# Kernel optimization log

Hardware: AMD Instinct MI355X
Metric: run time of the kernel (lower is better)

Reference implementation:

```python
import jax, jax.numpy as jnp
import numpy as np

N = 100000   # nodes
E = 640000   # edges
D = 128      # feature dim
G = 512      # graphs in the batch


def setup_inputs() -> dict:
    key = jax.random.key(0)
    ks = jax.random.split(key, 6)
    x = jax.random.normal(ks[0], (N, D), dtype=jnp.float32)
    edge_index = jax.random.randint(ks[1], (2, E), 0, N, dtype=jnp.int32)
    batch = jnp.sort(jax.random.randint(ks[2], (N,), 0, G, dtype=jnp.int32))
    scale = 1.0 / np.sqrt(D)
    W0 = jax.random.normal(ks[3], (D, D), dtype=jnp.float32) * scale
    W1 = jax.random.normal(ks[4], (D, D), dtype=jnp.float32) * scale
    W2 = jax.random.normal(ks[5], (D, D), dtype=jnp.float32) * scale
    return {"x": x, "edge_index": edge_index, "batch": batch,
            "W0": W0, "W1": W1, "W2": W2}


def gcn_conv(x, W, row, col, n):
    """GCNConv (bias=False): x' = D^-1/2 (A + I) D^-1/2 (x @ W).
    row/col already include self-loops."""
    xw = x @ W                                              # [N, D]
    deg = jax.ops.segment_sum(jnp.ones_like(col, dtype=x.dtype), col,
                              num_segments=n)               # [N]
    dinv = jnp.where(deg > 0, jax.lax.rsqrt(deg), 0.0)
    norm = dinv[row] * dinv[col]                            # [E+N]
    msgs = norm[:, None] * xw[row]                          # gather + scale
    return jax.ops.segment_sum(msgs, col, num_segments=n)   # scatter-add


def reference(x, edge_index, batch, W0, W1, W2):
    n = x.shape[0]
    loops = jnp.arange(n, dtype=edge_index.dtype)
    row = jnp.concatenate([edge_index[0], loops])
    col = jnp.concatenate([edge_index[1], loops])
    # conv_layers[:-1] (no activation between them in forward)
    x = gcn_conv(x, W0, row, col, n)
    x = gcn_conv(x, W1, row, col, n)
    x = jax.nn.leaky_relu(x, negative_slope=0.01)
    x = gcn_conv(x, W2, row, col, n)
    # global_add_pool over graph ids
    return jax.ops.segment_sum(x, batch, num_segments=G)    # [G, D]
```

## Files before the change

kernel.cpp:

```cpp
#include <hip/hip_runtime.h>
#include <hip/hip_bf16.h>

#define FEAT 128

typedef unsigned int uint32;
typedef unsigned short ushort16;
typedef __attribute__((ext_vector_type(8))) short short8;
typedef __attribute__((ext_vector_type(4))) float v4f;
typedef __attribute__((ext_vector_type(2))) float f32x2;

__device__ __forceinline__ ushort16 f2bf(float f) {
    uint32 u = __float_as_uint(f);
    u += 0x7fffu + ((u >> 16) & 1u);
    return (ushort16)(u >> 16);
}
__device__ __forceinline__ float bflo(uint32 u) { return __uint_as_float(u << 16); }
__device__ __forceinline__ float bfhi(uint32 u) { return __uint_as_float(u & 0xffff0000u); }
__device__ __forceinline__ f32x2 up2(uint32 u) { return (f32x2){bflo(u), bfhi(u)}; }

__device__ __forceinline__ void gemm_body(const float* __restrict__ A,
                                          const ushort16* __restrict__ Wt,
                                          ushort16* __restrict__ Ch, int n,
                                          int pairId, int pairStride,
                                          int tile0, int tile1, int t) {
    const int w = t >> 6;
    const int lane = t & 63;
    const int quad = lane >> 4;
    const int l16 = lane & 15;
    const int colBase = (w & 1) * 64;

    short8 wf[4][4];
#pragma unroll
    for (int ct = 0; ct < 4; ct++) {
        const ushort16* wp = Wt + (size_t)(colBase + ct * 16 + l16) * FEAT + quad * 8;
#pragma unroll
        for (int ks = 0; ks < 4; ks++) wf[ct][ks] = *(const short8*)(wp + ks * 32);
    }

    int tile = tile0 + pairId;
    if (tile >= tile1) return;

    auto loadA = [&](int tl, short8 (&a)[4]) {
        const int rowi = tl * 16 + l16;
        if (rowi < n) {
#pragma unroll
            for (int ks = 0; ks < 4; ks++) {
                const float* ap = A + (size_t)rowi * FEAT + quad * 8 + ks * 32;
                float4 f0 = *(const float4*)ap;
                float4 f1 = *(const float4*)(ap + 4);
                short8 v;
                v[0] = f2bf(f0.x); v[1] = f2bf(f0.y); v[2] = f2bf(f0.z); v[3] = f2bf(f0.w);
                v[4] = f2bf(f1.x); v[5] = f2bf(f1.y); v[6] = f2bf(f1.z); v[7] = f2bf(f1.w);
                a[ks] = v;
            }
        } else {
#pragma unroll
            for (int ks = 0; ks < 4; ks++) a[ks] = (short8)0;
        }
    };

    short8 aCur[4];
    loadA(tile, aCur);

    while (tile < tile1) {
        const int nextTile = tile + pairStride;
        short8 aNxt[4];
        if (nextTile < tile1) loadA(nextTile, aNxt);

        v4f acc[4];
#pragma unroll
        for (int ct = 0; ct < 4; ct++) acc[ct] = (v4f)0.f;
#pragma unroll
        for (int ct = 0; ct < 4; ct++)
#pragma unroll
            for (int ks = 0; ks < 4; ks++)
                acc[ct] = __builtin_amdgcn_mfma_f32_16x16x32_bf16(wf[ct][ks], aCur[ks], acc[ct], 0, 0, 0);

        const int rowi = tile * 16 + l16;
        if (rowi < n) {
#pragma unroll
            for (int ct = 0; ct < 4; ct++) {
                uint2 o;
                o.x = (uint32)f2bf(acc[ct][0]) | ((uint32)f2bf(acc[ct][1]) << 16);
                o.y = (uint32)f2bf(acc[ct][2]) | ((uint32)f2bf(acc[ct][3]) << 16);
                *(uint2*)(Ch + (size_t)rowi * FEAT + colBase + ct * 16 + quad * 4) = o;
            }
        }

        tile = nextTile;
#pragma unroll
        for (int ks = 0; ks < 4; ks++) aCur[ks] = aNxt[ks];
    }
}

__global__ __launch_bounds__(256) void pre_kernel(int* __restrict__ counts, int n,
                                                  const float* __restrict__ W0,
                                                  const float* __restrict__ W1,
                                                  ushort16* __restrict__ W01t,
                                                  float* __restrict__ Pbuf) {
    int b = blockIdx.x;
    int t = threadIdx.x;
    if (b < 100) {
        int idx = (b * 256 + t) * 4;
        if (idx + 3 < n) {
            *(int4*)(counts + idx) = make_int4(0, 0, 0, 0);
        } else {
            for (int i = idx; i < n; i++) counts[i] = 0;
        }
    } else if (b < 164) {
        __shared__ float sW0[2][FEAT];
        int wb = b - 100;
        int lk = t >> 7;
        int ncol = t & 127;
        int k = wb * 2 + lk;
        sW0[lk][ncol] = W0[(size_t)k * FEAT + ncol];
        __syncthreads();
        float acc = 0.f;
#pragma unroll 4
        for (int j = 0; j < FEAT; j++)
            acc += sW0[lk][j] * W1[(size_t)j * FEAT + ncol];
        W01t[(size_t)ncol * FEAT + k] = f2bf(acc);
    } else {
        int zb = b - 164;
        float4 z = make_float4(0.f, 0.f, 0.f, 0.f);
        float* p = Pbuf + (size_t)zb * 2048 + t * 8;
        *(float4*)p = z;
        *(float4*)(p + 4) = z;
    }
}

__global__ __launch_bounds__(256) void histgemmA_kernel(const int* __restrict__ col,
                                                        int* __restrict__ counts, int E,
                                                        const float* __restrict__ A,
                                                        const ushort16* __restrict__ Wt,
                                                        ushort16* __restrict__ Ch, int n) {
    const int b = blockIdx.x;
    const int r9 = b % 9;
    const int g9 = b / 9;
    const int t = threadIdx.x;
    if (r9 >= 4) {
        int hb = g9 * 5 + (r9 - 4);
        int id = hb * 256 + t;
        if (id * 4 + 3 < E) {
            int4 c4 = *(const int4*)(col + id * 4);
            atomicAdd(&counts[c4.x], 1);
            atomicAdd(&counts[c4.y], 1);
            atomicAdd(&counts[c4.z], 1);
            atomicAdd(&counts[c4.w], 1);
        } else {
            for (int e = id * 4; e < E; e++) atomicAdd(&counts[col[e]], 1);
        }
        return;
    }
    int gb = g9 * 4 + r9;
    gemm_body(A, Wt, Ch, n, gb * 2 + ((t >> 6) >> 1), 1024, 0, 3125, t);
}

__global__ __launch_bounds__(256) void scan_part(const int* __restrict__ counts,
                                                 int* __restrict__ bsum, int n) {
    __shared__ int s[256];
    int base = blockIdx.x * 1024;
    int t = threadIdx.x;
    int v = 0;
#pragma unroll
    for (int i = 0; i < 4; i++) {
        int idx = base + t * 4 + i;
        if (idx < n) v += counts[idx];
    }
    s[t] = v;
    __syncthreads();
    for (int o = 128; o > 0; o >>= 1) {
        if (t < o) s[t] += s[t + o];
        __syncthreads();
    }
    if (t == 0) bsum[blockIdx.x] = s[0];
}

__global__ __launch_bounds__(256) void scan_final(const int* __restrict__ counts,
                                                  const int* __restrict__ bsum,
                                                  int* __restrict__ off, int* __restrict__ nxt,
                                                  float* __restrict__ dinv, int n, int nb) {
    __shared__ int s[256];
    __shared__ int sb[128];
    int base = blockIdx.x * 1024;
    int t = threadIdx.x;
    if (t < nb) sb[t] = bsum[t];
    int c[4];
    int sum = 0;
#pragma unroll
    for (int i = 0; i < 4; i++) {
        int idx = base + t * 4 + i;
        c[i] = (idx < n) ? counts[idx] : 0;
        sum += c[i];
    }
    int v0 = sum;
    s[t] = sum;
    __syncthreads();
    for (int o = 1; o < 256; o <<= 1) {
        int v = (t >= o) ? s[t - o] : 0;
        __syncthreads();
        s[t] += v;
        __syncthreads();
    }
    int blockBase = 0;
    for (int j = 0; j < blockIdx.x; j++) blockBase += sb[j];
    int excl = s[t] - v0 + blockBase;
#pragma unroll
    for (int i = 0; i < 4; i++) {
        int idx = base + t * 4 + i;
        if (idx < n) {
            off[idx] = excl;
            nxt[idx] = excl;
            dinv[idx] = rsqrtf((float)(c[i] + 1));
        }
        excl += c[i];
    }
    if (blockIdx.x == gridDim.x - 1 && t == 255) off[n] = excl;
}

__global__ __launch_bounds__(256) void fillgemmB_kernel(const float* __restrict__ A,
                                                        const ushort16* __restrict__ Wt,
                                                        ushort16* __restrict__ Ch, int n,
                                                        const int* __restrict__ row,
                                                        const int* __restrict__ col,
                                                        int* __restrict__ nxt,
                                                        int* __restrict__ srcArr, int E) {
    const int b = blockIdx.x;
    const int r7 = b % 7;
    const int g7 = b / 7;
    const int t = threadIdx.x;
    if (r7 >= 2) {
        int fb = g7 * 5 + (r7 - 2);
        int e = fb * 256 + t;
        if (e < E) {
            int c = col[e], r = row[e];
            int p = atomicAdd(&nxt[c], 1);
            __builtin_nontemporal_store(r, &srcArr[p]);
        }
        return;
    }
    int gb = g7 * 2 + r7;
    gemm_body(A, Wt, Ch, n, gb * 2 + ((t >> 6) >> 1), 2048, 3125, 6250, t);
}

template <int MODE>
__global__ __launch_bounds__(256) void gather_kernel(const int* __restrict__ off,
                                                     const int* __restrict__ srcArr,
                                                     const float* __restrict__ dinv,
                                                     const uint4* __restrict__ table,
                                                     ushort16* __restrict__ Hh, int n) {
    const int t = threadIdx.x;
    const int node = blockIdx.x * 4 + (t >> 6);
    if (node >= n) return;
    const int lane = t & 63;
    const int grp = lane >> 4;
    const int l16 = lane & 15;
    float dc = dinv[node];

    f32x2 acc[4];
    if (grp == 0) {
        uint4 v = table[(size_t)node * 16 + l16];
        if (MODE == 0) {
            f32x2 w0 = (f32x2){dc, dc};
            acc[0] = w0 * up2(v.x);
            acc[1] = w0 * up2(v.y);
            acc[2] = w0 * up2(v.z);
            acc[3] = w0 * up2(v.w);
        } else {
            acc[0] = up2(v.x);
            acc[1] = up2(v.y);
            acc[2] = up2(v.z);
            acc[3] = up2(v.w);
        }
    } else {
#pragma unroll
        for (int j = 0; j < 4; j++) acc[j] = (f32x2){0.f, 0.f};
    }

    int s = off[node], e = off[node + 1];
    int i = s + grp;
    if (MODE == 0) {
        for (; i + 4 < e; i += 8) {
            int r0 = srcArr[i];
            int r1 = srcArr[i + 4];
            uint4 u0 = table[(size_t)r0 * 16 + l16];
            uint4 u1 = table[(size_t)r1 * 16 + l16];
            float f0 = dinv[r0];
            float f1 = dinv[r1];
            f32x2 n0 = (f32x2){f0, f0};
            f32x2 n1 = (f32x2){f1, f1};
            acc[0] += n0 * up2(u0.x);
            acc[1] += n0 * up2(u0.y);
            acc[2] += n0 * up2(u0.z);
            acc[3] += n0 * up2(u0.w);
            acc[0] += n1 * up2(u1.x);
            acc[1] += n1 * up2(u1.y);
            acc[2] += n1 * up2(u1.z);
            acc[3] += n1 * up2(u1.w);
        }
        if (i < e) {
            int r0 = srcArr[i];
            uint4 u0 = table[(size_t)r0 * 16 + l16];
            float f0 = dinv[r0];
            f32x2 n0 = (f32x2){f0, f0};
            acc[0] += n0 * up2(u0.x);
            acc[1] += n0 * up2(u0.y);
            acc[2] += n0 * up2(u0.z);
            acc[3] += n0 * up2(u0.w);
        }
    } else {
        for (; i + 4 < e; i += 8) {
            int r0 = srcArr[i];
            int r1 = srcArr[i + 4];
            uint4 u0 = table[(size_t)r0 * 16 + l16];
            uint4 u1 = table[(size_t)r1 * 16 + l16];
            acc[0] += up2(u0.x) + up2(u1.x);
            acc[1] += up2(u0.y) + up2(u1.y);
            acc[2] += up2(u0.z) + up2(u1.z);
            acc[3] += up2(u0.w) + up2(u1.w);
        }
        if (i < e) {
            int r0 = srcArr[i];
            uint4 u0 = table[(size_t)r0 * 16 + l16];
            acc[0] += up2(u0.x);
            acc[1] += up2(u0.y);
            acc[2] += up2(u0.z);
            acc[3] += up2(u0.w);
        }
    }

    float b[8] = {acc[0].x, acc[0].y, acc[1].x, acc[1].y,
                  acc[2].x, acc[2].y, acc[3].x, acc[3].y};
#pragma unroll
    for (int j = 0; j < 8; j++) {
        b[j] += __shfl_xor(b[j], 16);
        b[j] += __shfl_xor(b[j], 32);
    }

    if (grp == 0) {
        float sc = dc * dc;
        if (MODE == 1) {
#pragma unroll
            for (int j = 0; j < 8; j++) {
                float h = b[j];
                h = (h >= 0.f) ? h : 0.01f * h;
                b[j] = sc * h;
            }
        } else {
#pragma unroll
            for (int j = 0; j < 8; j++) b[j] *= sc;
        }
        uint4 o;
        o.x = (uint32)f2bf(b[0]) | ((uint32)f2bf(b[1]) << 16);
        o.y = (uint32)f2bf(b[2]) | ((uint32)f2bf(b[3]) << 16);
        o.z = (uint32)f2bf(b[4]) | ((uint32)f2bf(b[5]) << 16);
        o.w = (uint32)f2bf(b[6]) | ((uint32)f2bf(b[7]) << 16);
        *(uint4*)(Hh + (size_t)node * FEAT + l16 * 8) = o;
    }
}

__global__ __launch_bounds__(256) void gatherpool_kernel(const int* __restrict__ off,
                                                         const int* __restrict__ srcArr,
                                                         const float* __restrict__ dinv,
                                                         const uint4* __restrict__ table,
                                                         const int* __restrict__ batch,
                                                         float* __restrict__ P, int n) {
    const int t = threadIdx.x;
    const int wave = blockIdx.x * 4 + (t >> 6);
    const int lane = t & 63;
    const int grp = lane >> 4;
    const int l16 = lane & 15;

    const int node0 = wave * 16;
    if (node0 >= n) return;
    const int node1 = min(node0 + 16, n);

    float pacc[8];
#pragma unroll
    for (int j = 0; j < 8; j++) pacc[j] = 0.f;
    int cur = batch[node0];

    for (int node = node0; node < node1; node++) {
        float dc = dinv[node];
        f32x2 acc[4];
        if (grp == 0) {
            uint4 v = table[(size_t)node * 16 + l16];
            acc[0] = up2(v.x);
            acc[1] = up2(v.y);
            acc[2] = up2(v.z);
            acc[3] = up2(v.w);
        } else {
#pragma unroll
            for (int j = 0; j < 4; j++) acc[j] = (f32x2){0.f, 0.f};
        }

        int s = off[node], e = off[node + 1];
        int i = s + grp;
        for (; i + 4 < e; i += 8) {
            int r0 = srcArr[i];
            int r1 = srcArr[i + 4];
            uint4 u0 = table[(size_t)r0 * 16 + l16];
            uint4 u1 = table[(size_t)r1 * 16 + l16];
            acc[0] += up2(u0.x) + up2(u1.x);
            acc[1] += up2(u0.y) + up2(u1.y);
            acc[2] += up2(u0.z) + up2(u1.z);
            acc[3] += up2(u0.w) + up2(u1.w);
        }
        if (i < e) {
            int r0 = srcArr[i];
            uint4 u0 = table[(size_t)r0 * 16 + l16];
            acc[0] += up2(u0.x);
            acc[1] += up2(u0.y);
            acc[2] += up2(u0.z);
            acc[3] += up2(u0.w);
        }

        float b[8] = {acc[0].x, acc[0].y, acc[1].x, acc[1].y,
                      acc[2].x, acc[2].y, acc[3].x, acc[3].y};
#pragma unroll
        for (int j = 0; j < 8; j++) {
            b[j] += __shfl_xor(b[j], 16);
            b[j] += __shfl_xor(b[j], 32);
        }

        int g = batch[node];
        if (g != cur) {
            atomicAdd(&P[(size_t)cur * FEAT + l16 * 8 + 2 * grp], pacc[2 * grp]);
            atomicAdd(&P[(size_t)cur * FEAT + l16 * 8 + 2 * grp + 1], pacc[2 * grp + 1]);
#pragma unroll
            for (int j = 0; j < 8; j++) pacc[j] = 0.f;
            cur = g;
        }
#pragma unroll
        for (int j = 0; j < 8; j++) pacc[j] += dc * b[j];
    }
    atomicAdd(&P[(size_t)cur * FEAT + l16 * 8 + 2 * grp], pacc[2 * grp]);
    atomicAdd(&P[(size_t)cur * FEAT + l16 * 8 + 2 * grp + 1], pacc[2 * grp + 1]);
}

__global__ __launch_bounds__(128) void pgemm_kernel(const float* __restrict__ P,
                                                    const float* __restrict__ W2,
                                                    float* __restrict__ out) {
    __shared__ float sP[FEAT];
    const int g = blockIdx.x;
    const int t = threadIdx.x;
    sP[t] = P[(size_t)g * FEAT + t];
    __syncthreads();
    float o = 0.f;
#pragma unroll 4
    for (int k = 0; k < FEAT; k++) o += sP[k] * W2[(size_t)k * FEAT + t];
    out[(size_t)g * FEAT + t] = o;
}

extern "C" void kernel_launch(void* const* d_in, const int* in_sizes, int n_in,
                              void* d_out, int out_size, void* d_ws, size_t ws_size,
                              hipStream_t stream) {
    const float* x = (const float*)d_in[0];
    const int* ei = (const int*)d_in[1];
    const int* batch = (const int*)d_in[2];
    const float* W0 = (const float*)d_in[3];
    const float* W1 = (const float*)d_in[4];
    const float* W2 = (const float*)d_in[5];
    float* out = (float*)d_out;

    const int N = in_sizes[0] / FEAT;
    const int E = in_sizes[1] / 2;
    const int G = out_size / FEAT;

    const int* rowI = ei;
    const int* colI = ei + E;

    char* ws = (char*)d_ws;
    auto take = [&](size_t bytes) {
        char* p = ws;
        ws += (bytes + 15) & ~(size_t)15;
        return p;
    };
    int* counts    = (int*)take((size_t)N * 4);
    int* off       = (int*)take((size_t)(N + 1) * 4);
    int* nxt       = (int*)take((size_t)N * 4);
    float* dinv    = (float*)take((size_t)N * 4);
    int* bsum      = (int*)take(128 * 4);
    int* srcArr    = (int*)take((size_t)E * 4);
    ushort16* W01t = (ushort16*)take((size_t)16384 * 2);
    float* Pbuf    = (float*)take((size_t)G * FEAT * 4);
    ushort16* bufA = (ushort16*)take((size_t)N * FEAT * 2);
    ushort16* bufB = (ushort16*)take((size_t)N * FEAT * 2);

    const int nb = (N + 1023) / 1024;

    pre_kernel<<<196, 256, 0, stream>>>(counts, N, W0, W1, W01t, Pbuf);

    histgemmA_kernel<<<128 * 9, 256, 0, stream>>>(colI, counts, E, x, W01t, bufA, N);

    scan_part<<<nb, 256, 0, stream>>>(counts, bsum, N);
    scan_final<<<nb, 256, 0, stream>>>(counts, bsum, off, nxt, dinv, N, nb);

    fillgemmB_kernel<<<512 * 7, 256, 0, stream>>>(x, W01t, bufA, N,
                                                  rowI, colI, nxt, srcArr, E);

    const int gatBlocks = (N + 3) / 4;
    gather_kernel<0><<<gatBlocks, 256, 0, stream>>>(off, srcArr, dinv,
                                                    (const uint4*)bufA, bufB, N);
    gather_kernel<1><<<gatBlocks, 256, 0, stream>>>(off, srcArr, dinv,
                                                    (const uint4*)bufB, bufA, N);
    const int nWaves = (N + 15) / 16;
    const int poolBlocks = (nWaves + 3) / 4;
    gatherpool_kernel<<<poolBlocks, 256, 0, stream>>>(off, srcArr, dinv,
                                                      (const uint4*)bufA, batch,
                                                      Pbuf, N);
    pgemm_kernel<<<G, 128, 0, stream>>>(Pbuf, W2, out);
}
```

Measured before the change: 327.1 us.

## Fuse tail gathers into cooperative persistent kernel and chain-scan offsets

Replaces the two-kernel scan with a single decoupled chained scan: each block publishes its total through a flag array and the earlier blocks' totals are summed by spinning. The two gather passes, the pooled gather and the final small GEMM are merged into one cooperative persistent kernel of 2048 blocks, with grid-wide syncs in place of separate launches. The aim is to remove launch gaps and tail idle time between the small dependent stages. In exchange it adds grid-sync costs and a grid-stride loop. The chained scan relies on earlier blocks being scheduled first, and the fused path depends on the cooperative launch succeeding, with the old kernels kept as a fallback.

Result: slower. 1.075 ms (+228.5%).

```diff
diff --git a/kernel.cpp b/kernel.cpp
--- a/kernel.cpp
+++ b/kernel.cpp
@@ -1,5 +1,8 @@
 #include <hip/hip_runtime.h>
 #include <hip/hip_bf16.h>
+#include <hip/hip_cooperative_groups.h>
+
+namespace cg = cooperative_groups;
 
 #define FEAT 128
 
@@ -97,7 +100,8 @@
                                                   const float* __restrict__ W0,
                                                   const float* __restrict__ W1,
                                                   ushort16* __restrict__ W01t,
-                                                  float* __restrict__ Pbuf) {
+                                                  float* __restrict__ Pbuf,
+                                                  int* __restrict__ flagval) {
     int b = blockIdx.x;
     int t = threadIdx.x;
     if (b < 100) {
@@ -120,12 +124,14 @@
         for (int j = 0; j < FEAT; j++)
             acc += sW0[lk][j] * W1[(size_t)j * FEAT + ncol];
         W01t[(size_t)ncol * FEAT + k] = f2bf(acc);
-    } else {
+    } else if (b < 196) {
         int zb = b - 164;
         float4 z = make_float4(0.f, 0.f, 0.f, 0.f);
         float* p = Pbuf + (size_t)zb * 2048 + t * 8;
         *(float4*)p = z;
         *(float4*)(p + 4) = z;
+    } else {
+        if (t < 128) flagval[t] = 0;
     }
 }
 
@@ -156,35 +162,15 @@
     gemm_body(A, Wt, Ch, n, gb * 2 + ((t >> 6) >> 1), 1024, 0, 3125, t);
 }
 
-__global__ __launch_bounds__(256) void scan_part(const int* __restrict__ counts,
-                                                 int* __restrict__ bsum, int n) {
+__global__ __launch_bounds__(256) void scan_chain(const int* __restrict__ counts,
+                                                  int* __restrict__ flagval,
+                                                  int* __restrict__ off, int* __restrict__ nxt,
+                                                  float* __restrict__ dinv, int n) {
     __shared__ int s[256];
-    int base = blockIdx.x * 1024;
-    int t = threadIdx.x;
-    int v = 0;
-#pragma unroll
-    for (int i = 0; i < 4; i++) {
-        int idx = base + t * 4 + i;
-        if (idx < n) v += counts[idx];
-    }
-    s[t] = v;
-    __syncthreads();
-    for (int o = 128; o > 0; o >>= 1) {
-        if (t < o) s[t] += s[t + o];
-        __syncthreads();
-    }
-    if (t == 0) bsum[blockIdx.x] = s[0];
-}
-
-__global__ __launch_bounds__(256) void scan_final(const int* __restrict__ counts,
-                                                  const int* __restrict__ bsum,
-                                                  int* __restrict__ off, int* __restrict__ nxt,
-                                                  float* __restrict__ dinv, int n, int nb) {
-    __shared__ int s[256];
-    __shared__ int sb[128];
-    int base = blockIdx.x * 1024;
-    int t = threadIdx.x;
-    if (t < nb) sb[t] = bsum[t];
+    __shared__ int sBase;
+    const int b = blockIdx.x;
+    const int base = b * 1024;
+    const int t = threadIdx.x;
     int c[4];
     int sum = 0;
 #pragma unroll
@@ -202,9 +188,18 @@
         s[t] += v;
         __syncthreads();
     }
-    int blockBase = 0;
-    for (int j = 0; j < blockIdx.x; j++) blockBase += sb[j];
-    int excl = s[t] - v0 + blockBase;
+    if (t == 255) atomicExch(&flagval[b], s[255] + 1);
+    if (t == 0) {
+        int acc = 0;
+        for (int j = 0; j < b; j++) {
+            int v;
+            do { v = atomicAdd(&flagval[j], 0); } while (v == 0);
+            acc += v - 1;
+        }
+        sBase = acc;
+    }
+    __syncthreads();
+    int excl = s[t] - v0 + sBase;
 #pragma unroll
     for (int i = 0; i < 4; i++) {
         int idx = base + t * 4 + i;
@@ -215,7 +210,7 @@
         }
         excl += c[i];
     }
-    if (blockIdx.x == gridDim.x - 1 && t == 255) off[n] = excl;
+    if (b == gridDim.x - 1 && t == 255) off[n] = excl;
 }
 
 __global__ __launch_bounds__(256) void fillgemmB_kernel(const float* __restrict__ A,
@@ -244,19 +239,13 @@
 }
 
 template <int MODE>
-__global__ __launch_bounds__(256) void gather_kernel(const int* __restrict__ off,
-                                                     const int* __restrict__ srcArr,
-                                                     const float* __restrict__ dinv,
-                                                     const uint4* __restrict__ table,
-                                                     ushort16* __restrict__ Hh, int n) {
-    const int t = threadIdx.x;
-    const int node = blockIdx.x * 4 + (t >> 6);
-    if (node >= n) return;
-    const int lane = t & 63;
-    const int grp = lane >> 4;
-    const int l16 = lane & 15;
+__device__ __forceinline__ void gather_node_body(int node, int grp, int l16,
+                                                 const int* __restrict__ off,
+                                                 const int* __restrict__ srcArr,
+                                                 const float* __restrict__ dinv,
+                                                 const uint4* __restrict__ table,
+                                                 ushort16* __restrict__ Hh) {
     float dc = dinv[node];
-
     f32x2 acc[4];
     if (grp == 0) {
         uint4 v = table[(size_t)node * 16 + l16];
@@ -359,20 +348,14 @@
     }
 }
 
-__global__ __launch_bounds__(256) void gatherpool_kernel(const int* __restrict__ off,
-                                                         const int* __restrict__ srcArr,
-                                                         const float* __restrict__ dinv,
-                                                         const uint4* __restrict__ table,
-                                                         const int* __restrict__ batch,
-                                                         float* __restrict__ P, int n) {
-    const int t = threadIdx.x;
-    const int wave = blockIdx.x * 4 + (t >> 6);
-    const int lane = t & 63;
-    const int grp = lane >> 4;
-    const int l16 = lane & 15;
-
+__device__ __forceinline__ void gatherpool_wave(int wave, int grp, int l16,
+                                                const int* __restrict__ off,
+                                                const int* __restrict__ srcArr,
+                                                const float* __restrict__ dinv,
+                                                const uint4* __restrict__ table,
+                                                const int* __restrict__ batch,
+                                                float* __restrict__ P, int n) {
     const int node0 = wave * 16;
-    if (node0 >= n) return;
     const int node1 = min(node0 + 16, n);
 
     float pacc[8];
@@ -438,18 +421,87 @@
     atomicAdd(&P[(size_t)cur * FEAT + l16 * 8 + 2 * grp + 1], pacc[2 * grp + 1]);
 }
 
+__device__ __forceinline__ void pgemm_graph(int g, int t,
+                                            const float* __restrict__ P,
+                                            const float* __restrict__ W2,
+                                            float* __restrict__ out) {
+    __shared__ float sP[FEAT];
+    if (t < FEAT) sP[t] = P[(size_t)g * FEAT + t];
+    __syncthreads();
+    if (t < FEAT) {
+        float o = 0.f;
+#pragma unroll 4
+        for (int k = 0; k < FEAT; k++) o += sP[k] * W2[(size_t)k * FEAT + t];
+        out[(size_t)g * FEAT + t] = o;
+    }
+    __syncthreads();
+}
+
+template <int MODE>
+__global__ __launch_bounds__(256) void gather_kernel(const int* __restrict__ off,
+                                                     const int* __restrict__ srcArr,
+                                                     const float* __restrict__ dinv,
+                                                     const uint4* __restrict__ table,
+                                                     ushort16* __restrict__ Hh, int n) {
+    const int t = threadIdx.x;
+    const int node = blockIdx.x * 4 + (t >> 6);
+    if (node >= n) return;
+    gather_node_body<MODE>(node, (t & 63) >> 4, t & 15, off, srcArr, dinv, table, Hh);
+}
+
+__global__ __launch_bounds__(256) void gatherpool_kernel(const int* __restrict__ off,
+                                                         const int* __restrict__ srcArr,
+                                                         const float* __restrict__ dinv,
+                                                         const uint4* __restrict__ table,
+                                                         const int* __restrict__ batch,
+                                                         float* __restrict__ P, int n) {
+    const int t = threadIdx.x;
+    const int wave = blockIdx.x * 4 + (t >> 6);
+    if (wave * 16 >= n) return;
+    gatherpool_wave(wave, (t & 63) >> 4, t & 15, off, srcArr, dinv, table, batch, P, n);
+}
+
 __global__ __launch_bounds__(128) void pgemm_kernel(const float* __restrict__ P,
                                                     const float* __restrict__ W2,
                                                     float* __restrict__ out) {
-    __shared__ float sP[FEAT];
-    const int g = blockIdx.x;
+    pgemm_graph(blockIdx.x, threadIdx.x, P, W2, out);
+}
+
+__global__ __launch_bounds__(256, 8) void tail_kernel(const int* __restrict__ off,
+                                                      const int* __restrict__ srcArr,
+                                                      const float* __restrict__ dinv,
+                                                      ushort16* __restrict__ bufA,
+                                                      ushort16* __restrict__ bufB,
+                                                      const int* __restrict__ batch,
+                                                      float* __restrict__ P,
+                                                      const float* __restrict__ W2,
+                                                      float* __restrict__ out,
+                                                      int n, int G) {
+    cg::grid_group grid = cg::this_grid();
     const int t = threadIdx.x;
-    sP[t] = P[(size_t)g * FEAT + t];
-    __syncthreads();
-    float o = 0.f;
-#pragma unroll 4
-    for (int k = 0; k < FEAT; k++) o += sP[k] * W2[(size_t)k * FEAT + t];
-    out[(size_t)g * FEAT + t] = o;
+    const int grp = (t & 63) >> 4;
+    const int l16 = t & 15;
+
+    for (int q = blockIdx.x; q * 4 < n; q += gridDim.x) {
+        int node = q * 4 + (t >> 6);
+        if (node < n)
+            gather_node_body<0>(node, grp, l16, off, srcArr, dinv,
+                                (const uint4*)bufA, bufB);
+    }
+    grid.sync();
+    for (int q = blockIdx.x; q * 4 < n; q += gridDim.x) {
+        int node = q * 4 + (t >> 6);
+        if (node < n)
+            gather_node_body<1>(node, grp, l16, off, srcArr, dinv,
+                                (const uint4*)bufB, bufA);
+    }
+    grid.sync();
+    for (int wave = blockIdx.x * 4 + (t >> 6); wave * 16 < n; wave += gridDim.x * 4)
+        gatherpool_wave(wave, grp, l16, off, srcArr, dinv,
+                        (const uint4*)bufA, batch, P, n);
+    grid.sync();
+    for (int g = blockIdx.x; g < G; g += gridDim.x)
+        pgemm_graph(g, t, P, W2, out);
 }
 
 extern "C" void kernel_launch(void* const* d_in, const int* in_sizes, int n_in,
@@ -480,7 +532,7 @@
     int* off       = (int*)take((size_t)(N + 1) * 4);
     int* nxt       = (int*)take((size_t)N * 4);
     float* dinv    = (float*)take((size_t)N * 4);
-    int* bsum      = (int*)take(128 * 4);
+    int* flagval   = (int*)take(128 * 4);
     int* srcArr    = (int*)take((size_t)E * 4);
     ushort16* W01t = (ushort16*)take((size_t)16384 * 2);
     float* Pbuf    = (float*)take((size_t)G * FEAT * 4);
@@ -489,25 +541,36 @@
 
     const int nb = (N + 1023) / 1024;
 
-    pre_kernel<<<196, 256, 0, stream>>>(counts, N, W0, W1, W01t, Pbuf);
+    pre_kernel<<<197, 256, 0, stream>>>(counts, N, W0, W1, W01t, Pbuf, flagval);
 
     histgemmA_kernel<<<128 * 9, 256, 0, stream>>>(colI, counts, E, x, W01t, bufA, N);
 
-    scan_part<<<nb, 256, 0, stream>>>(counts, bsum, N);
-    scan_final<<<nb, 256, 0, stream>>>(counts, bsum, off, nxt, dinv, N, nb);
+    scan_chain<<<nb, 256, 0, stream>>>(counts, flagval, off, nxt, dinv, N);
 
     fillgemmB_kernel<<<512 * 7, 256, 0, stream>>>(x, W01t, bufA, N,
                                                   rowI, colI, nxt, srcArr, E);
 
-    const int gatBlocks = (N + 3) / 4;
-    gather_kernel<0><<<gatBlocks, 256, 0, stream>>>(off, srcArr, dinv,
-                                                    (const uint4*)bufA, bufB, N);
-    gather_kernel<1><<<gatBlocks, 256, 0, stream>>>(off, srcArr, dinv,
-                                                    (const uint4*)bufB, bufA, N);
-    const int nWaves = (N + 15) / 16;
-    const int poolBlocks = (nWaves + 3) / 4;
-    gatherpool_kernel<<<poolBlocks, 256, 0, stream>>>(off, srcArr, dinv,
-                                                      (const uint4*)bufA, batch,
-                                                      Pbuf, N);
-    pgemm_kernel<<<G, 128, 0, stream>>>(Pbuf, W2, out);
-}
+    {
+        int Nv = N, Gv = G;
+        void* args[] = {(void*)&off, (void*)&srcArr, (void*)&dinv,
+                        (void*)&bufA, (void*)&bufB, (void*)&batch,
+                        (void*)&Pbuf, (void*)&W2, (void*)&out,
+                        (void*)&Nv, (void*)&Gv};
+        hipError_t cerr = hipLaunchCooperativeKernel((void*)tail_kernel,
+                                                     dim3(2048), dim3(256),
+                                                     args, 0, stream);
+        if (cerr != hipSuccess) {
+            const int gatBlocks = (N + 3) / 4;
+            gather_kernel<0><<<gatBlocks, 256, 0, stream>>>(off, srcArr, dinv,
+                                                            (const uint4*)bufA, bufB, N);
+            gather_kernel<1><<<gatBlocks, 256, 0, stream>>>(off, srcArr, dinv,
+                                                            (const uint4*)bufB, bufA, N);
+            const int nWaves = (N + 15) / 16;
+            const int poolBlocks = (nWaves + 3) / 4;
+            gatherpool_kernel<<<poolBlocks, 256, 0, stream>>>(off, srcArr, dinv,
+                                                              (const uint4*)bufA, batch,
+                                                              Pbuf, N);
+            pgemm_kernel<<<G, 128, 0, stream>>>(Pbuf, W2, out);
+        }
+    }
+}
```
